# Performance work log

Measured on AMD Instinct MI355X. Metric: run time of the kernel, lower is better.

The kernel has to match this reference:

```python
import jax, jax.numpy as jnp
import numpy as np
from jax import lax

E = 256


def _channel_attention(x, avg_w, avg_b, max_w, max_b):
    # x: [b,1,N]; 1x1 conv on a [b,1,1,1] tensor is a scalar affine map
    avg = jnp.mean(x, axis=-1, keepdims=True)          # [b,1,1]
    mx = jnp.max(x, axis=-1, keepdims=True)            # [b,1,1]
    a = jax.nn.relu(avg_w[0, 0, 0, 0] * avg + avg_b[0])
    m = jax.nn.relu(max_w[0, 0, 0, 0] * mx + max_b[0])
    return a + m                                        # [b,1,1]


def _spatial_attention(x, sp_w, sp_b):
    # x: [b,1,1]; torch .repeat(1,2,1,1) on a 3D tensor -> [1, 2b, 1, 1]
    x4 = jnp.tile(x[None], (1, 2, 1, 1))                # [1,2b,1,1]
    avg = jnp.mean(x4, axis=1, keepdims=True)           # [1,1,1,1]
    mx = jnp.max(x4, axis=1, keepdims=True)             # [1,1,1,1]
    cat = jnp.concatenate([avg, mx], axis=1)            # [1,2,1,1]
    out = lax.conv_general_dilated(cat, sp_w, (1, 1), [(3, 3), (3, 3)])
    return jax.nn.relu(out + sp_b.reshape(1, 1, 1, 1))  # [1,1,1,1]


def _mha(q_in, k_in, v_in, in_w, in_b, out_w, out_b):
    # torch nn.MultiheadAttention, seq-first layout [L, N, E], num_heads=1
    wq, wk, wv = in_w[:E], in_w[E:2 * E], in_w[2 * E:]
    bq, bk, bv = in_b[:E], in_b[E:2 * E], in_b[2 * E:]
    q = q_in @ wq.T + bq
    k = k_in @ wk.T + bk
    v = v_in @ wv.T + bv                                 # [L,N,E]
    scores = jnp.einsum('lne,mne->nlm', q, k) / jnp.sqrt(jnp.float32(E))
    attn = jax.nn.softmax(scores, axis=-1)               # [N,L,L]
    o = jnp.einsum('nlm,mne->lne', attn, v)              # [L,N,E]
    return o @ out_w.T + out_b


def _gru_cell(x, h, w_ih, w_hh, b_ih, b_hh):
    gi = x @ w_ih.T + b_ih
    gh = h @ w_hh.T + b_hh
    ir, iz, in_ = gi[..., :E], gi[..., E:2 * E], gi[..., 2 * E:]
    hr, hz, hn = gh[..., :E], gh[..., E:2 * E], gh[..., 2 * E:]
    r = jax.nn.sigmoid(ir + hr)
    z = jax.nn.sigmoid(iz + hz)
    n = jnp.tanh(in_ + r * hn)
    return (1.0 - z) * n + z * h


def _ssf(x, ssf_w, ssf_b):
    # x: [b,s,e] -> unsqueeze channel, 7x7 conv, relu -> [b,1,s,e]
    out = lax.conv_general_dilated(x[:, None], ssf_w, (1, 1), [(3, 3), (3, 3)])
    return jax.nn.relu(out + ssf_b.reshape(1, 1, 1, 1))


def setup_inputs() -> dict:
    key = jax.random.key(0)
    ks = jax.random.split(key, 20)
    B, S = 32, 2048
    p = lambda k, shape: jax.random.normal(k, shape, jnp.float32) * 0.05
    return {
        'text_feature': jax.random.normal(ks[0], (B, S, E), jnp.float32),
        'graph_feature': jax.random.normal(ks[1], (B, S, E), jnp.float32),
        'avg_w': p(ks[2], (1, 1, 1, 1)), 'avg_b': p(ks[3], (1,)),
        'max_w': p(ks[4], (1, 1, 1, 1)), 'max_b': p(ks[5], (1,)),
        'sp_w': p(ks[6], (1, 2, 7, 7)), 'sp_b': p(ks[7], (1,)),
        'in_proj_w': p(ks[8], (3 * E, E)), 'in_proj_b': p(ks[9], (3 * E,)),
        'out_w': p(ks[10], (E, E)), 'out_b': p(ks[11], (E,)),
        'lin_w': p(ks[12], (E, E)), 'lin_b': p(ks[13], (E,)),
        'w_ih': p(ks[14], (3 * E, E)), 'w_hh': p(ks[15], (3 * E, E)),
        'b_ih': p(ks[16], (3 * E,)), 'b_hh': p(ks[17], (3 * E,)),
        'ssf_w': p(ks[18], (1, 1, 7, 7)), 'ssf_b': p(ks[19], (1,)),
    }


def reference(text_feature, graph_feature, avg_w, avg_b, max_w, max_b,
              sp_w, sp_b, in_proj_w, in_proj_b, out_w, out_b,
              lin_w, lin_b, w_ih, w_hh, b_ih, b_hh, ssf_w, ssf_b):
    b, s, e = text_feature.shape
    tf4 = text_feature[:, None]                           # [b,1,s,e]
    gf4 = graph_feature[:, None]
    tf_flat = tf4.reshape(b, 1, -1)                       # [b,1,s*e]
    gf_flat = gf4.reshape(b, 1, -1)

    tf_c = _channel_attention(tf_flat, avg_w, avg_b, max_w, max_b)  # [b,1,1]
    gf_c = _channel_attention(gf_flat, avg_w, avg_b, max_w, max_b)

    cross = tf_c @ jnp.swapaxes(gf_c, 1, 2)               # [b,1,1]
    tf_cw = jax.nn.softmax(cross, axis=-1) @ tf_c         # [b,1,1]
    gf_cw = jax.nn.softmax(jnp.swapaxes(cross, 1, 2), axis=-1) @ gf_c

    tf_s = _spatial_attention(tf_cw, sp_w, sp_b)          # [1,1,1,1]
    gf_s = _spatial_attention(gf_cw, sp_w, sp_b)
    norm_tf = jax.nn.softmax(tf_s, axis=2)                # ones (size-1 axis)
    norm_gf = jax.nn.softmax(gf_s, axis=2)

    tf_fused = (tf4 + norm_tf * tf4).reshape(b, s, e)
    gf_fused = (gf4 + norm_gf * gf4).reshape(b, s, e)

    # ESA (fixed call semantics): shared MHA, cross keys
    tf_att = _mha(tf_fused, gf_fused, tf_fused, in_proj_w, in_proj_b, out_w, out_b)
    gf_att = _mha(gf_fused, tf_fused, gf_fused, in_proj_w, in_proj_b, out_w, out_b)

    inter = (tf_att * gf_att) @ lin_w.T + lin_b           # [b,s,e]
    g_tf = _gru_cell(inter, tf_att, w_ih, w_hh, b_ih, b_hh)
    g_gf = _gru_cell(inter, gf_att, w_ih, w_hh, b_ih, b_hh)

    return _ssf(g_tf, ssf_w, ssf_b) + _ssf(g_gf, ssf_w, ssf_b)  # [b,1,s,e]
```

## Files before the change

kernel.cpp:

```cpp
#include <hip/hip_runtime.h>

typedef unsigned short u16;
typedef short s16x8 __attribute__((ext_vector_type(8)));
typedef float f32x4 __attribute__((ext_vector_type(4)));

#define DEVI static __device__ __forceinline__
#define MFMA16(A, B, C) __builtin_amdgcn_mfma_f32_16x16x32_bf16(A, B, C, 0, 0, 0)
#define Z4 ((f32x4){0.f, 0.f, 0.f, 0.f})

DEVI float bf2f(u16 u) {
  __bf16 h; __builtin_memcpy(&h, &u, 2); return (float)h;
}
DEVI u16 f2bf(float f) {
  __bf16 h = (__bf16)f;
  u16 u; __builtin_memcpy(&u, &h, 2); return u;
}
DEVI float rcpf_(float x) { return __builtin_amdgcn_rcpf(x); }
DEVI float sigmoidf_(float x) { return rcpf_(1.0f + __expf(-x)); }
DEVI float tanhf_(float x) { return 1.0f - 2.0f * rcpf_(__expf(2.0f * x) + 1.0f); }

__global__ void k_wconv(const float* __restrict__ w0, const float* __restrict__ w1,
                        const float* __restrict__ w2, const float* __restrict__ w3,
                        const float* __restrict__ w4, u16* __restrict__ out) {
  int c = blockIdx.x * 256 + threadIdx.x;
  if (c >= 90112) return;
  const float* src; long base; int cl;
  if (c < 24576)      { src = w0; base = 0;      cl = c; }
  else if (c < 32768) { src = w1; base = 196608; cl = c - 24576; }
  else if (c < 40960) { src = w2; base = 262144; cl = c - 32768; }
  else if (c < 65536) { src = w3; base = 327680; cl = c - 40960; }
  else                { src = w4; base = 524288; cl = c - 65536; }
  int lr = cl & 15, kg = (cl >> 4) & 3, ks = (cl >> 6) & 7, ct = cl >> 9;
  const float* sp = src + (ct * 16 + lr) * 256 + ks * 32 + kg * 8;
  f32x4 v0 = *(const f32x4*)sp;
  f32x4 v1 = *(const f32x4*)(sp + 4);
  s16x8 t;
  t[0] = (short)f2bf(v0[0]); t[1] = (short)f2bf(v0[1]);
  t[2] = (short)f2bf(v0[2]); t[3] = (short)f2bf(v0[3]);
  t[4] = (short)f2bf(v1[0]); t[5] = (short)f2bf(v1[1]);
  t[6] = (short)f2bf(v1[2]); t[7] = (short)f2bf(v1[3]);
  *(s16x8*)(out + base + (long)cl * 8) = t;
}

__global__ void k_tr(const float* __restrict__ text, const float* __restrict__ graph,
                     u16* __restrict__ T2T, u16* __restrict__ T2G) {
  long idx = (long)blockIdx.x * 256 + threadIdx.x;
  int side = (int)(idx >> 21);
  long r = (idx >> 5) & 65535;
  int c8 = (int)(idx & 31);
  long b = r >> 11, s = r & 2047;
  const float* src = (side ? graph : text) + r * 256 + c8 * 8;
  u16* dst = (side ? T2G : T2T) + ((s << 5) + b) * 256 + c8 * 8;
  f32x4 v0 = *(const f32x4*)src;
  f32x4 v1 = *(const f32x4*)(src + 4);
  s16x8 t;
  t[0] = (short)f2bf(2.f * v0[0]); t[1] = (short)f2bf(2.f * v0[1]);
  t[2] = (short)f2bf(2.f * v0[2]); t[3] = (short)f2bf(2.f * v0[3]);
  t[4] = (short)f2bf(2.f * v1[0]); t[5] = (short)f2bf(2.f * v1[1]);
  t[6] = (short)f2bf(2.f * v1[2]); t[7] = (short)f2bf(2.f * v1[3]);
  *(s16x8*)dst = t;
}

#define AOo 0
#define AXo 8448
#define KBo 16896
#define QBo 25344
#define SFo 33792
#define PBo 35904
#define VTo 8448
#define OBo 25344
#define STo 16896

__global__ __launch_bounds__(256, 2) void k_attn(
    const u16* __restrict__ T2T, const u16* __restrict__ T2G,
    const u16* __restrict__ Wproj, const float* __restrict__ bproj,
    const u16* __restrict__ Wout, const float* __restrict__ bout,
    u16* __restrict__ attT, u16* __restrict__ attG) {
  __shared__ u16 sh[37184];
  int n = blockIdx.x, s = blockIdx.y;
  const u16* pown = (s ? T2G : T2T) + n * 8192;
  const u16* poth = (s ? T2T : T2G) + n * 8192;
  u16* dst = s ? attG : attT;
  int tid = threadIdx.x, w = tid >> 6, lane = tid & 63;
  int lr = lane & 15, kg = lane >> 4;
  int fro = ((kg << 4) + lr) * 8;

  {
    int r = tid >> 3, c0 = (tid & 7) * 32;
    const u16* so = pown + r * 256 + c0;
    const u16* sx = poth + r * 256 + c0;
    u16* d0 = sh + AOo + r * 264 + c0;
    u16* d1 = sh + AXo + r * 264 + c0;
#pragma unroll
    for (int j = 0; j < 4; ++j) {
      *(s16x8*)(d0 + j * 8) = *(const s16x8*)(so + j * 8);
      *(s16x8*)(d1 + j * 8) = *(const s16x8*)(sx + j * 8);
    }
  }
  __syncthreads();

  s16x8 af[2][8];

#pragma unroll
  for (int mt = 0; mt < 2; ++mt)
#pragma unroll
    for (int k = 0; k < 8; ++k)
      af[mt][k] = *(const s16x8*)(sh + AXo + (mt * 16 + lr) * 264 + k * 32 + kg * 8);
  for (int i = 0; i < 4; ++i) {
    int ct = 16 + w * 4 + i;
    const u16* wp = Wproj + (ct << 12) + fro;
    s16x8 b[8];
#pragma unroll
    for (int k = 0; k < 8; ++k) b[k] = *(const s16x8*)(wp + (k << 9));
    f32x4 a0 = Z4, a1 = Z4;
#pragma unroll
    for (int k = 0; k < 8; ++k) {
      a0 = MFMA16(af[0][k], b[k], a0);
      a1 = MFMA16(af[1][k], b[k], a1);
    }
    int colk = (ct << 4) + lr;
    float bias = bproj[colk];
    u16* base = sh + KBo + (colk - 256);
#pragma unroll
    for (int j = 0; j < 4; ++j) {
      base[(kg * 4 + j) * 264] = f2bf(a0[j] + bias);
      base[(16 + kg * 4 + j) * 264] = f2bf(a1[j] + bias);
    }
  }

#pragma unroll
  for (int mt = 0; mt < 2; ++mt)
#pragma unroll
    for (int k = 0; k < 8; ++k)
      af[mt][k] = *(const s16x8*)(sh + AOo + (mt * 16 + lr) * 264 + k * 32 + kg * 8);
  for (int i = 0; i < 4; ++i) {
    int ct = w * 4 + i;
    const u16* wp = Wproj + (ct << 12) + fro;
    s16x8 b[8];
#pragma unroll
    for (int k = 0; k < 8; ++k) b[k] = *(const s16x8*)(wp + (k << 9));
    f32x4 a0 = Z4, a1 = Z4;
#pragma unroll
    for (int k = 0; k < 8; ++k) {
      a0 = MFMA16(af[0][k], b[k], a0);
      a1 = MFMA16(af[1][k], b[k], a1);
    }
    int colq = (ct << 4) + lr;
    float bias = bproj[colq];
    u16* base = sh + QBo + colq;
#pragma unroll
    for (int j = 0; j < 4; ++j) {
      base[(kg * 4 + j) * 264] = f2bf(a0[j] + bias);
      base[(16 + kg * 4 + j) * 264] = f2bf(a1[j] + bias);
    }
  }
  __syncthreads();

  {
    int mt = w >> 1, nt = w & 1;
    f32x4 acc = Z4;
#pragma unroll
    for (int k = 0; k < 8; ++k) {
      s16x8 qa = *(const s16x8*)(sh + QBo + (mt * 16 + lr) * 264 + k * 32 + kg * 8);
      s16x8 kb = *(const s16x8*)(sh + KBo + (nt * 16 + lr) * 264 + k * 32 + kg * 8);
      acc = MFMA16(qa, kb, acc);
    }
    float* Sf = (float*)(sh + SFo);
#pragma unroll
    for (int j = 0; j < 4; ++j)
      Sf[(mt * 16 + kg * 4 + j) * 33 + nt * 16 + lr] = acc[j] * 0.0625f;
  }
  __syncthreads();

  for (int i = 0; i < 4; ++i) {
    int ct = 32 + w * 4 + i;
    const u16* wp = Wproj + (ct << 12) + fro;
    s16x8 b[8];
#pragma unroll
    for (int k = 0; k < 8; ++k) b[k] = *(const s16x8*)(wp + (k << 9));
    f32x4 a0 = Z4, a1 = Z4;
#pragma unroll
    for (int k = 0; k < 8; ++k) {
      a0 = MFMA16(af[0][k], b[k], a0);
      a1 = MFMA16(af[1][k], b[k], a1);
    }
    int colv = (ct << 4) + lr;
    float bias = bproj[colv];
    u16* base = sh + VTo + (colv - 512) * 40;
#pragma unroll
    for (int j = 0; j < 4; ++j) {
      base[kg * 4 + j] = f2bf(a0[j] + bias);
      base[16 + kg * 4 + j] = f2bf(a1[j] + bias);
    }
  }
  if (tid < 32) {
    float* Sp = (float*)(sh + SFo) + tid * 33;
    float mx = -1e30f;
#pragma unroll
    for (int m = 0; m < 32; ++m) mx = fmaxf(mx, Sp[m]);
    float e[32]; float sum = 0.f;
#pragma unroll
    for (int m = 0; m < 32; ++m) { e[m] = __expf(Sp[m] - mx); sum += e[m]; }
    float inv = rcpf_(sum);
    u16* Pp = sh + PBo + tid * 40;
#pragma unroll
    for (int m = 0; m < 32; ++m) Pp[m] = f2bf(e[m] * inv);
  }
  __syncthreads();

  {
    s16x8 pa0 = *(const s16x8*)(sh + PBo + lr * 40 + kg * 8);
    s16x8 pa1 = *(const s16x8*)(sh + PBo + (16 + lr) * 40 + kg * 8);
#pragma unroll
    for (int i = 0; i < 4; ++i) {
      int e0 = (w * 4 + i) * 16;
      s16x8 vb = *(const s16x8*)(sh + VTo + (e0 + lr) * 40 + kg * 8);
      f32x4 a0 = MFMA16(pa0, vb, Z4);
      f32x4 a1 = MFMA16(pa1, vb, Z4);
      u16* base = sh + OBo + e0 + lr;
#pragma unroll
      for (int j = 0; j < 4; ++j) {
        base[(kg * 4 + j) * 264] = f2bf(a0[j]);
        base[(16 + kg * 4 + j) * 264] = f2bf(a1[j]);
      }
    }
  }
  __syncthreads();

  {
    s16x8 ao[2][8];
#pragma unroll
    for (int mt = 0; mt < 2; ++mt)
#pragma unroll
      for (int k = 0; k < 8; ++k)
        ao[mt][k] = *(const s16x8*)(sh + OBo + (mt * 16 + lr) * 264 + k * 32 + kg * 8);
    for (int i = 0; i < 4; ++i) {
      int ct = w * 4 + i;
      const u16* wp = Wout + (ct << 12) + fro;
      s16x8 b[8];
#pragma unroll
      for (int k = 0; k < 8; ++k) b[k] = *(const s16x8*)(wp + (k << 9));
      f32x4 a0 = Z4, a1 = Z4;
#pragma unroll
      for (int k = 0; k < 8; ++k) {
        a0 = MFMA16(ao[0][k], b[k], a0);
        a1 = MFMA16(ao[1][k], b[k], a1);
      }
      int cb = (ct << 4) + lr;
      float bias = bout[cb];
      u16* base = sh + STo + cb;
#pragma unroll
      for (int j = 0; j < 4; ++j) {
        base[(kg * 4 + j) * 264] = f2bf(a0[j] + bias);
        base[(16 + kg * 4 + j) * 264] = f2bf(a1[j] + bias);
      }
    }
  }
  __syncthreads();
  {
    int r = tid >> 3, c0 = (tid & 7) * 32;
    u16* dr = dst + ((long)r * 2048 + n) * 256 + c0;
#pragma unroll
    for (int j = 0; j < 4; ++j)
      *(s16x8*)(dr + j * 8) = *(const s16x8*)(sh + STo + r * 264 + c0 + j * 8);
  }
}

__global__ __launch_bounds__(512, 1) void k_gru(
    const u16* __restrict__ attT, const u16* __restrict__ attG,
    const u16* __restrict__ Wlin, const float* __restrict__ blin,
    const u16* __restrict__ Wih, const float* __restrict__ bih,
    const u16* __restrict__ Whh, const float* __restrict__ bhh,
    u16* __restrict__ g1, u16* __restrict__ g2) {
  __shared__ u16 sh[25344];
  const int AT = 0, AG = 8448, HI = 16896;
  int m0 = blockIdx.x * 32;
  int tid = threadIdx.x, w = tid >> 6, lane = tid & 63;
  int lr = lane & 15, kg = lane >> 4;
  int fro = ((kg << 4) + lr) * 8;

  {
    int r = tid >> 4, c0 = (tid & 15) * 16;
    const u16* pt = attT + (m0 + r) * 256 + c0;
    const u16* pg = attG + (m0 + r) * 256 + c0;
    *(s16x8*)(sh + AT + r * 264 + c0) = __builtin_nontemporal_load((const s16x8*)pt);
    *(s16x8*)(sh + AT + r * 264 + c0 + 8) = __builtin_nontemporal_load((const s16x8*)(pt + 8));
    *(s16x8*)(sh + AG + r * 264 + c0) = __builtin_nontemporal_load((const s16x8*)pg);
    *(s16x8*)(sh + AG + r * 264 + c0 + 8) = __builtin_nontemporal_load((const s16x8*)(pg + 8));
  }
  __syncthreads();

  s16x8 aH[2][8];
#pragma unroll
  for (int mt = 0; mt < 2; ++mt)
#pragma unroll
    for (int k = 0; k < 8; ++k) {
      s16x8 t8 = *(const s16x8*)(sh + AT + (mt * 16 + lr) * 264 + k * 32 + kg * 8);
      s16x8 g8 = *(const s16x8*)(sh + AG + (mt * 16 + lr) * 264 + k * 32 + kg * 8);
      s16x8 h;
#pragma unroll
      for (int j = 0; j < 8; ++j)
        h[j] = (short)f2bf(bf2f((u16)t8[j]) * bf2f((u16)g8[j]));
      aH[mt][k] = h;
    }

#pragma unroll
  for (int ic = 0; ic < 2; ++ic) {
    int ct = w * 2 + ic;
    const u16* wp = Wlin + (ct << 12) + fro;
    s16x8 bw[2];
    bw[0] = *(const s16x8*)(wp);
    f32x4 a0 = Z4, a1 = Z4;
#pragma unroll
    for (int k = 0; k < 8; ++k) {
      const int c = k & 1, nx = c ^ 1;
      if (k < 7) bw[nx] = *(const s16x8*)(wp + ((k + 1) << 9));
      a0 = MFMA16(aH[0][k], bw[c], a0);
      a1 = MFMA16(aH[1][k], bw[c], a1);
    }
    int col = (ct << 4) + lr;
    float bias = blin[col];
    u16* base = sh + HI + col;
#pragma unroll
    for (int j = 0; j < 4; ++j) {
      base[(kg * 4 + j) * 264] = f2bf(a0[j] + bias);
      base[(16 + kg * 4 + j) * 264] = f2bf(a1[j] + bias);
    }
  }
  __syncthreads();

#define LDGATE(slot, kk) { \
    int fo_ = ((kk) << 9) + fro; \
    bI[slot][0] = *(const s16x8*)(Wih + (ct0 << 12) + fo_); \
    bI[slot][1] = *(const s16x8*)(Wih + (ct1 << 12) + fo_); \
    bI[slot][2] = *(const s16x8*)(Wih + (ct2 << 12) + fo_); \
    bH[slot][0] = *(const s16x8*)(Whh + (ct0 << 12) + fo_); \
    bH[slot][1] = *(const s16x8*)(Whh + (ct1 << 12) + fo_); \
    bH[slot][2] = *(const s16x8*)(Whh + (ct2 << 12) + fo_); }

  s16x8 o1b[2], o2b[2];
#pragma unroll
  for (int ic = 0; ic < 2; ++ic) {
    int ct0 = w * 2 + ic, ct1 = 16 + ct0, ct2 = 32 + ct0;
    int col = (ct0 << 4) + lr;
    f32x4 acc[3][3][2];
#pragma unroll
    for (int g = 0; g < 3; ++g)
#pragma unroll
      for (int s2 = 0; s2 < 3; ++s2) { acc[g][s2][0] = Z4; acc[g][s2][1] = Z4; }
    s16x8 bI[2][3], bH[2][3];
    LDGATE(0, 0)
#pragma unroll
    for (int k = 0; k < 8; ++k) {
      const int c = k & 1, nx = c ^ 1;
      if (k < 7) { LDGATE(nx, k + 1) }
      int ko = k * 32 + kg * 8;
      s16x8 aI0 = *(const s16x8*)(sh + HI + lr * 264 + ko);
      s16x8 aI1 = *(const s16x8*)(sh + HI + (16 + lr) * 264 + ko);
      s16x8 aT0 = *(const s16x8*)(sh + AT + lr * 264 + ko);
      s16x8 aT1 = *(const s16x8*)(sh + AT + (16 + lr) * 264 + ko);
      s16x8 aG0 = *(const s16x8*)(sh + AG + lr * 264 + ko);
      s16x8 aG1 = *(const s16x8*)(sh + AG + (16 + lr) * 264 + ko);
#pragma unroll
      for (int g = 0; g < 3; ++g) {
        acc[g][0][0] = MFMA16(aI0, bI[c][g], acc[g][0][0]);
        acc[g][0][1] = MFMA16(aI1, bI[c][g], acc[g][0][1]);
        acc[g][1][0] = MFMA16(aT0, bH[c][g], acc[g][1][0]);
        acc[g][1][1] = MFMA16(aT1, bH[c][g], acc[g][1][1]);
        acc[g][2][0] = MFMA16(aG0, bH[c][g], acc[g][2][0]);
        acc[g][2][1] = MFMA16(aG1, bH[c][g], acc[g][2][1]);
      }
    }
    float bir = bih[col], biz = bih[col + 256], bin_ = bih[col + 512];
    float bhr = bhh[col], bhz = bhh[col + 256], bhn = bhh[col + 512];
    s16x8 o1v, o2v;
#pragma unroll
    for (int mt = 0; mt < 2; ++mt)
#pragma unroll
      for (int j = 0; j < 4; ++j) {
        int row = mt * 16 + kg * 4 + j;
        float hT = bf2f(sh[AT + row * 264 + col]);
        float hG = bf2f(sh[AG + row * 264 + col]);
        float ir = acc[0][0][mt][j] + bir;
        float iz = acc[1][0][mt][j] + biz;
        float inn = acc[2][0][mt][j] + bin_;
        float r1 = sigmoidf_(ir + acc[0][1][mt][j] + bhr);
        float z1 = sigmoidf_(iz + acc[1][1][mt][j] + bhz);
        float n1 = tanhf_(inn + r1 * (acc[2][1][mt][j] + bhn));
        o1v[mt * 4 + j] = (short)f2bf((1.f - z1) * n1 + z1 * hT);
        float r2 = sigmoidf_(ir + acc[0][2][mt][j] + bhr);
        float z2 = sigmoidf_(iz + acc[1][2][mt][j] + bhz);
        float n2 = tanhf_(inn + r2 * (acc[2][2][mt][j] + bhn));
        o2v[mt * 4 + j] = (short)f2bf((1.f - z2) * n2 + z2 * hG);
      }
    o1b[ic] = o1v; o2b[ic] = o2v;
  }
  __syncthreads();

#pragma unroll
  for (int ic = 0; ic < 2; ++ic) {
    int col = ((w * 2 + ic) << 4) + lr;
#pragma unroll
    for (int mt = 0; mt < 2; ++mt)
#pragma unroll
      for (int j = 0; j < 4; ++j) {
        int row = mt * 16 + kg * 4 + j;
        sh[AT + row * 264 + col] = (u16)o1b[ic][mt * 4 + j];
        sh[AG + row * 264 + col] = (u16)o2b[ic][mt * 4 + j];
      }
  }
  __syncthreads();
  {
    int r = tid >> 4, c0 = (tid & 15) * 16;
    u16* p1 = g1 + (long)(m0 + r) * 256 + c0;
    u16* p2 = g2 + (long)(m0 + r) * 256 + c0;
    *(s16x8*)(p1) = *(const s16x8*)(sh + AT + r * 264 + c0);
    *(s16x8*)(p1 + 8) = *(const s16x8*)(sh + AT + r * 264 + c0 + 8);
    *(s16x8*)(p2) = *(const s16x8*)(sh + AG + r * 264 + c0);
    *(s16x8*)(p2 + 8) = *(const s16x8*)(sh + AG + r * 264 + c0 + 8);
  }
}

__global__ __launch_bounds__(256) void k_conv(
    const u16* __restrict__ g1, const u16* __restrict__ g2,
    const float* __restrict__ wss, const float* __restrict__ bss,
    float* __restrict__ out) {
  __shared__ float s1[38][73];
  __shared__ float s2[38][73];
  int et = blockIdx.x, st = blockIdx.y, b = blockIdx.z;
  int s0 = st * 32, e0 = et * 64;
  int tid = threadIdx.x;
  for (int idx = tid; idx < 38 * 70; idx += 256) {
    int r = idx / 70, c = idx % 70;
    int s = s0 + r - 3, e = e0 + c - 3;
    float v1 = 0.f, v2 = 0.f;
    if (s >= 0 && s < 2048 && e >= 0 && e < 256) {
      long off = ((long)b * 2048 + s) * 256 + e;
      v1 = bf2f(g1[off]); v2 = bf2f(g2[off]);
    }
    s1[r][c] = v1; s2[r][c] = v2;
  }
  __syncthreads();
  float bias = bss[0];
  int oy = tid >> 3, ox = (tid & 7) * 8;
  float a1[8] = {0.f, 0.f, 0.f, 0.f, 0.f, 0.f, 0.f, 0.f};
  float a2[8] = {0.f, 0.f, 0.f, 0.f, 0.f, 0.f, 0.f, 0.f};
#pragma unroll
  for (int ky = 0; ky < 7; ++ky) {
    float wr[7];
#pragma unroll
    for (int kx = 0; kx < 7; ++kx) wr[kx] = wss[ky * 7 + kx];
    float r1[14], r2[14];
#pragma unroll
    for (int j = 0; j < 14; ++j) { r1[j] = s1[oy + ky][ox + j]; r2[j] = s2[oy + ky][ox + j]; }
#pragma unroll
    for (int x = 0; x < 8; ++x)
#pragma unroll
      for (int kx = 0; kx < 7; ++kx) {
        a1[x] += r1[x + kx] * wr[kx];
        a2[x] += r2[x + kx] * wr[kx];
      }
  }
  long obase = ((long)b * 2048 + s0 + oy) * 256 + e0 + ox;
  f32x4 o0, o1;
#pragma unroll
  for (int x = 0; x < 4; ++x) {
    o0[x] = fmaxf(a1[x] + bias, 0.f) + fmaxf(a2[x] + bias, 0.f);
    o1[x] = fmaxf(a1[x + 4] + bias, 0.f) + fmaxf(a2[x + 4] + bias, 0.f);
  }
  *(f32x4*)(out + obase) = o0;
  *(f32x4*)(out + obase + 4) = o1;
}

extern "C" void kernel_launch(void* const* d_in, const int* in_sizes, int n_in,
                              void* d_out, int out_size, void* d_ws, size_t ws_size,
                              hipStream_t stream) {
  const float* text = (const float*)d_in[0];
  const float* graph = (const float*)d_in[1];
  const float* in_proj_w = (const float*)d_in[8];
  const float* in_proj_b = (const float*)d_in[9];
  const float* out_w = (const float*)d_in[10];
  const float* out_b = (const float*)d_in[11];
  const float* lin_w = (const float*)d_in[12];
  const float* lin_b = (const float*)d_in[13];
  const float* w_ih = (const float*)d_in[14];
  const float* w_hh = (const float*)d_in[15];
  const float* b_ih = (const float*)d_in[16];
  const float* b_hh = (const float*)d_in[17];
  const float* ssf_w = (const float*)d_in[18];
  const float* ssf_b = (const float*)d_in[19];

  u16* g1 = (u16*)d_ws;
  u16* g2 = g1 + 16777216;
  u16* T2T = g1;
  u16* T2G = g2;
  u16* Wall = g2 + 16777216;
  u16* Wproj = Wall;
  u16* Wout = Wall + 196608;
  u16* Wlin = Wall + 262144;
  u16* Wih = Wall + 327680;
  u16* Whh = Wall + 524288;

  u16* attT = (u16*)d_out;
  u16* attG = attT + 16777216;

  k_wconv<<<352, 256, 0, stream>>>(in_proj_w, out_w, lin_w, w_ih, w_hh, Wall);
  k_tr<<<16384, 256, 0, stream>>>(text, graph, T2T, T2G);

  k_attn<<<dim3(2048, 2), 256, 0, stream>>>(T2T, T2G, Wproj, in_proj_b, Wout, out_b, attT, attG);
  k_gru<<<2048, 512, 0, stream>>>(attT, attG, Wlin, lin_b, Wih, b_ih, Whh, b_hh, g1, g2);
  k_conv<<<dim3(4, 64, 32), 256, 0, stream>>>(g1, g2, ssf_w, ssf_b, (float*)d_out);
}
```

Measured before the change: 391.3 us.

## Fold linear layer into GRU input weights and write attention output seq-major

```diff
diff --git a/kernel.cpp b/kernel.cpp
--- a/kernel.cpp
+++ b/kernel.cpp
@@ -20,16 +20,13 @@
 DEVI float tanhf_(float x) { return 1.0f - 2.0f * rcpf_(__expf(2.0f * x) + 1.0f); }
 
 __global__ void k_wconv(const float* __restrict__ w0, const float* __restrict__ w1,
-                        const float* __restrict__ w2, const float* __restrict__ w3,
                         const float* __restrict__ w4, u16* __restrict__ out) {
   int c = blockIdx.x * 256 + threadIdx.x;
-  if (c >= 90112) return;
+  if (c >= 57344) return;
   const float* src; long base; int cl;
   if (c < 24576)      { src = w0; base = 0;      cl = c; }
   else if (c < 32768) { src = w1; base = 196608; cl = c - 24576; }
-  else if (c < 40960) { src = w2; base = 262144; cl = c - 32768; }
-  else if (c < 65536) { src = w3; base = 327680; cl = c - 40960; }
-  else                { src = w4; base = 524288; cl = c - 65536; }
+  else                { src = w4; base = 458752; cl = c - 32768; }
   int lr = cl & 15, kg = (cl >> 4) & 3, ks = (cl >> 6) & 7, ct = cl >> 9;
   const float* sp = src + (ct * 16 + lr) * 256 + ks * 32 + kg * 8;
   f32x4 v0 = *(const f32x4*)sp;
@@ -40,6 +37,29 @@
   t[4] = (short)f2bf(v1[0]); t[5] = (short)f2bf(v1[1]);
   t[6] = (short)f2bf(v1[2]); t[7] = (short)f2bf(v1[3]);
   *(s16x8*)(out + base + (long)cl * 8) = t;
+}
+
+__global__ __launch_bounds__(256) void k_wcomb(
+    const float* __restrict__ w_ih, const float* __restrict__ lin_w,
+    const float* __restrict__ b_lin, const float* __restrict__ b_ih,
+    u16* __restrict__ outw, float* __restrict__ outb) {
+  __shared__ float row[256];
+  int i = blockIdx.x;
+  int tid = threadIdx.x;
+  row[tid] = w_ih[i * 256 + tid];
+  __syncthreads();
+  float acc = 0.f;
+#pragma unroll 8
+  for (int o = 0; o < 256; ++o) acc += row[o] * lin_w[o * 256 + tid];
+  int ct = i >> 4, lr = i & 15;
+  int ks = tid >> 5, kg = (tid >> 3) & 3, jj = tid & 7;
+  long cl = (ct * 8 + ks) * 64 + kg * 16 + lr;
+  outw[cl * 8 + jj] = f2bf(acc);
+  if (tid == 0) {
+    float s = 0.f;
+    for (int o = 0; o < 256; ++o) s += row[o] * b_lin[o];
+    outb[i] = s + b_ih[i];
+  }
 }
 
 __global__ void k_tr(const float* __restrict__ text, const float* __restrict__ graph,
@@ -259,7 +279,7 @@
   __syncthreads();
   {
     int r = tid >> 3, c0 = (tid & 7) * 32;
-    u16* dr = dst + ((long)r * 2048 + n) * 256 + c0;
+    u16* dr = dst + ((long)n << 13) + r * 256 + c0;
 #pragma unroll
     for (int j = 0; j < 4; ++j)
       *(s16x8*)(dr + j * 8) = *(const s16x8*)(sh + STo + r * 264 + c0 + j * 8);
@@ -268,12 +288,11 @@
 
 __global__ __launch_bounds__(512, 1) void k_gru(
     const u16* __restrict__ attT, const u16* __restrict__ attG,
-    const u16* __restrict__ Wlin, const float* __restrict__ blin,
-    const u16* __restrict__ Wih, const float* __restrict__ bih,
+    const u16* __restrict__ Wcomb, const float* __restrict__ bcomb,
     const u16* __restrict__ Whh, const float* __restrict__ bhh,
     u16* __restrict__ g1, u16* __restrict__ g2) {
-  __shared__ u16 sh[25344];
-  const int AT = 0, AG = 8448, HI = 16896;
+  __shared__ u16 sh[16896];
+  const int AT = 0, AG = 8448;
   int m0 = blockIdx.x * 32;
   int tid = threadIdx.x, w = tid >> 6, lane = tid & 63;
   int lr = lane & 15, kg = lane >> 4;
@@ -304,36 +323,11 @@
       aH[mt][k] = h;
     }
 
-#pragma unroll
-  for (int ic = 0; ic < 2; ++ic) {
-    int ct = w * 2 + ic;
-    const u16* wp = Wlin + (ct << 12) + fro;
-    s16x8 bw[2];
-    bw[0] = *(const s16x8*)(wp);
-    f32x4 a0 = Z4, a1 = Z4;
-#pragma unroll
-    for (int k = 0; k < 8; ++k) {
-      const int c = k & 1, nx = c ^ 1;
-      if (k < 7) bw[nx] = *(const s16x8*)(wp + ((k + 1) << 9));
-      a0 = MFMA16(aH[0][k], bw[c], a0);
-      a1 = MFMA16(aH[1][k], bw[c], a1);
-    }
-    int col = (ct << 4) + lr;
-    float bias = blin[col];
-    u16* base = sh + HI + col;
-#pragma unroll
-    for (int j = 0; j < 4; ++j) {
-      base[(kg * 4 + j) * 264] = f2bf(a0[j] + bias);
-      base[(16 + kg * 4 + j) * 264] = f2bf(a1[j] + bias);
-    }
-  }
-  __syncthreads();
-
 #define LDGATE(slot, kk) { \
     int fo_ = ((kk) << 9) + fro; \
-    bI[slot][0] = *(const s16x8*)(Wih + (ct0 << 12) + fo_); \
-    bI[slot][1] = *(const s16x8*)(Wih + (ct1 << 12) + fo_); \
-    bI[slot][2] = *(const s16x8*)(Wih + (ct2 << 12) + fo_); \
+    bI[slot][0] = *(const s16x8*)(Wcomb + (ct0 << 12) + fo_); \
+    bI[slot][1] = *(const s16x8*)(Wcomb + (ct1 << 12) + fo_); \
+    bI[slot][2] = *(const s16x8*)(Wcomb + (ct2 << 12) + fo_); \
     bH[slot][0] = *(const s16x8*)(Whh + (ct0 << 12) + fo_); \
     bH[slot][1] = *(const s16x8*)(Whh + (ct1 << 12) + fo_); \
     bH[slot][2] = *(const s16x8*)(Whh + (ct2 << 12) + fo_); }
@@ -355,23 +349,21 @@
       const int c = k & 1, nx = c ^ 1;
       if (k < 7) { LDGATE(nx, k + 1) }
       int ko = k * 32 + kg * 8;
-      s16x8 aI0 = *(const s16x8*)(sh + HI + lr * 264 + ko);
-      s16x8 aI1 = *(const s16x8*)(sh + HI + (16 + lr) * 264 + ko);
       s16x8 aT0 = *(const s16x8*)(sh + AT + lr * 264 + ko);
       s16x8 aT1 = *(const s16x8*)(sh + AT + (16 + lr) * 264 + ko);
       s16x8 aG0 = *(const s16x8*)(sh + AG + lr * 264 + ko);
       s16x8 aG1 = *(const s16x8*)(sh + AG + (16 + lr) * 264 + ko);
 #pragma unroll
       for (int g = 0; g < 3; ++g) {
-        acc[g][0][0] = MFMA16(aI0, bI[c][g], acc[g][0][0]);
-        acc[g][0][1] = MFMA16(aI1, bI[c][g], acc[g][0][1]);
+        acc[g][0][0] = MFMA16(aH[0][k], bI[c][g], acc[g][0][0]);
+        acc[g][0][1] = MFMA16(aH[1][k], bI[c][g], acc[g][0][1]);
         acc[g][1][0] = MFMA16(aT0, bH[c][g], acc[g][1][0]);
         acc[g][1][1] = MFMA16(aT1, bH[c][g], acc[g][1][1]);
         acc[g][2][0] = MFMA16(aG0, bH[c][g], acc[g][2][0]);
         acc[g][2][1] = MFMA16(aG1, bH[c][g], acc[g][2][1]);
       }
     }
-    float bir = bih[col], biz = bih[col + 256], bin_ = bih[col + 512];
+    float bir = bcomb[col], biz = bcomb[col + 256], bin_ = bcomb[col + 512];
     float bhr = bhh[col], bhz = bhh[col + 256], bhn = bhh[col + 512];
     s16x8 o1v, o2v;
 #pragma unroll
@@ -435,7 +427,7 @@
     int s = s0 + r - 3, e = e0 + c - 3;
     float v1 = 0.f, v2 = 0.f;
     if (s >= 0 && s < 2048 && e >= 0 && e < 256) {
-      long off = ((long)b * 2048 + s) * 256 + e;
+      long off = ((long)s * 32 + b) * 256 + e;
       v1 = bf2f(g1[off]); v2 = bf2f(g2[off]);
     }
     s1[r][c] = v1; s2[r][c] = v2;
@@ -497,17 +489,18 @@
   u16* Wall = g2 + 16777216;
   u16* Wproj = Wall;
   u16* Wout = Wall + 196608;
-  u16* Wlin = Wall + 262144;
-  u16* Wih = Wall + 327680;
-  u16* Whh = Wall + 524288;
+  u16* Wcomb = Wall + 262144;
+  u16* Whh = Wall + 458752;
+  float* bcomb = (float*)(Wall + 655360);
 
   u16* attT = (u16*)d_out;
   u16* attG = attT + 16777216;
 
-  k_wconv<<<352, 256, 0, stream>>>(in_proj_w, out_w, lin_w, w_ih, w_hh, Wall);
+  k_wconv<<<224, 256, 0, stream>>>(in_proj_w, out_w, w_hh, Wall);
+  k_wcomb<<<768, 256, 0, stream>>>(w_ih, lin_w, lin_b, b_ih, Wcomb, bcomb);
   k_tr<<<16384, 256, 0, stream>>>(text, graph, T2T, T2G);
 
   k_attn<<<dim3(2048, 2), 256, 0, stream>>>(T2T, T2G, Wproj, in_proj_b, Wout, out_b, attT, attG);
-  k_gru<<<2048, 512, 0, stream>>>(attT, attG, Wlin, lin_b, Wih, b_ih, Whh, b_hh, g1, g2);
+  k_gru<<<2048, 512, 0, stream>>>(attT, attG, Wcomb, bcomb, Whh, b_hh, g1, g2);
   k_conv<<<dim3(4, 64, 32), 256, 0, stream>>>(g1, g2, ssf_w, ssf_b, (float*)d_out);
 }
```

After: 488.2 us. +24.8%, slower.
